# Kernel optimization log

Hardware: AMD Instinct MI355X
Metric: run time of the kernel (lower is better)

## Reference

```python
import jax, jax.numpy as jnp
import numpy as np

B, D, N, H = 16384, 8, 64, 128   # batch, input_path_dim, cde_state_dim, vf_hidden_dim
NSIG = D + D * (D - 1) // 2       # Lyndon words up to depth 2: letters + pairs i<j


def setup_inputs() -> dict:
    key = jax.random.key(0)
    ks = jax.random.split(key, 6)
    g = lambda k, shape, scale: jax.random.normal(k, shape, jnp.float32) * scale
    return {
        "h": jax.random.normal(ks[0], (B, N), jnp.float32),
        "primitive_signature": jax.random.normal(ks[1], (B, NSIG), jnp.float32) * 0.1,
        "W1": g(ks[2], (H, N), (1.0 / N) ** 0.5),
        "b1": jnp.zeros((H,), jnp.float32),
        "W2": g(ks[3], (H, H), (1.0 / H) ** 0.5),
        "b2": jnp.zeros((H,), jnp.float32),
        "W3": g(ks[4], (D * N, H), (1.0 / H) ** 0.5),
        "b3": jnp.zeros((D * N,), jnp.float32),
    }


def reference(h, primitive_signature, W1, b1, W2, b2, W3, b3):
    d, n = D, N
    iu, ju = np.triu_indices(d, k=1)  # level-2 Lyndon words ij with i<j, lex order

    def vf(hv):  # MLP vector field: (n,) -> (d, n), one field per input channel
        z = jax.nn.softplus(W1 @ hv + b1)
        z = jax.nn.softplus(W2 @ z + b2)
        return jnp.tanh(W3 @ z + b3).reshape(d, n)

    def single(hv, sig):
        V = vf(hv)  # (d, n) level-1 brackets (the vector fields themselves)
        # JVP of the whole stacked field in direction t: J_{V_j}(h) @ t for all j
        jvp_dir = lambda t: jax.jvp(vf, (hv,), (t,))[1]  # (d, n)
        JV = jax.vmap(jvp_dir)(V)                         # (i, j, n) = J_{V_j} V_i
        # Lie bracket [V_i, V_j](h) = J_{V_j} V_i - J_{V_i} V_j
        br2 = JV - jnp.swapaxes(JV, 0, 1)                 # (i, j, n)
        lyn2 = br2[iu, ju]                                # (d*(d-1)/2, n)
        # log-ODE contraction: sum_w logsig_w * bracket_w(h)
        return sig[:d] @ V + sig[d:] @ lyn2               # (n,)

    return jax.vmap(single)(h, primitive_signature)
```

## Files before the change

### kernel.cpp

```cpp
#include <hip/hip_runtime.h>
#include <hip/hip_bf16.h>

#define NEL 16384

#define W1B_OFF 0
#define W2B_OFF 8192
#define W3B_OFF 24576
#define WS_WEIGHTS 90112
#define S1_OFF  90112
#define S2_OFF  (S1_OFF + NEL*128)
#define Z2_OFF  (S2_OFF + NEL*128)
#define V_OFF   (Z2_OFF + NEL*128)
#define DZ1_OFF (V_OFF + NEL*512)
#define DZ2_OFF (DZ1_OFF + NEL*8*128)

typedef __attribute__((ext_vector_type(8))) short bf16x8;
typedef __attribute__((ext_vector_type(4))) float f32x4;

__device__ __forceinline__ float bf2f(unsigned int u16) {
    unsigned int x = u16 << 16;
    float f; __builtin_memcpy(&f, &x, 4); return f;
}
__device__ __forceinline__ unsigned short f2bf(float f) {
    unsigned int x; __builtin_memcpy(&x, &f, 4);
    x = (x + 0x7FFFu + ((x >> 16) & 1u)) >> 16;
    return (unsigned short)x;
}
__device__ __forceinline__ void unpack8(uint4 q, float* f) {
    f[0] = bf2f(q.x & 0xFFFFu); f[1] = bf2f(q.x >> 16);
    f[2] = bf2f(q.y & 0xFFFFu); f[3] = bf2f(q.y >> 16);
    f[4] = bf2f(q.z & 0xFFFFu); f[5] = bf2f(q.z >> 16);
    f[6] = bf2f(q.w & 0xFFFFu); f[7] = bf2f(q.w >> 16);
}
__device__ __forceinline__ void sp_sig(float x, float& sp, float& sig) {
    float t = __expf(-fabsf(x));
    float r = __builtin_amdgcn_rcpf(1.f + t);
    sig = (x >= 0.f) ? r : 1.f - r;
    sp  = fmaxf(x, 0.f) + __logf(1.f + t);
}
__device__ __forceinline__ float tanh_fast(float x) {
    float t = __expf(-2.f * fabsf(x));
    float y = (1.f - t) * __builtin_amdgcn_rcpf(1.f + t);
    unsigned int xb, yb;
    __builtin_memcpy(&xb, &x, 4);
    __builtin_memcpy(&yb, &y, 4);
    yb |= (xb & 0x80000000u);
    float rr; __builtin_memcpy(&rr, &yb, 4);
    return rr;
}
__device__ __forceinline__ bf16x8 ldfrag(const unsigned short* p) {
    return *reinterpret_cast<const bf16x8*>(p);
}
__device__ __forceinline__ void cpu4(unsigned short* dst, const unsigned short* src) {
    *reinterpret_cast<uint4*>(dst) = *reinterpret_cast<const uint4*>(src);
}

__global__ void prep_weights(const float* __restrict__ W1,
                             const float* __restrict__ W2,
                             const float* __restrict__ W3,
                             unsigned short* __restrict__ wb) {
    int i = blockIdx.x * blockDim.x + threadIdx.x;
    if (i >= WS_WEIGHTS) return;
    float v;
    if (i < W2B_OFF) v = W1[i];
    else if (i < W3B_OFF) v = W2[i - W2B_OFF];
    else v = W3[i - W3B_OFF];
    wb[i] = f2bf(v);
}

#define K1_LDS 39168
__global__ __launch_bounds__(256, 4)
void k1_fwd12(const float* __restrict__ hg,
              const float* __restrict__ b1,
              const float* __restrict__ b2,
              unsigned short* __restrict__ wsb) {
    __shared__ __align__(16) char sm[K1_LDS];
    unsigned short* w1s = (unsigned short*)(sm);
    unsigned short* hs  = (unsigned short*)(sm + 18432);
    unsigned short* w2s = (unsigned short*)(sm);
    unsigned short* z1s = (unsigned short*)(sm + 34816);
    unsigned short* S1g = wsb + S1_OFF;
    unsigned short* S2g = wsb + S2_OFF;
    unsigned short* Z2g = wsb + Z2_OFF;

    const int tid = threadIdx.x;
    const int e0 = blockIdx.x * 16;
    const int lane = tid & 63;
    const int w = tid >> 6;
    const int r16 = lane & 15;
    const int kb = lane >> 4;
    const int crow = kb * 4;

    #pragma unroll
    for (int q = 0; q < 4; ++q) {
        int idx = q * 256 + tid;
        int row = idx >> 3, u4 = idx & 7;
        cpu4(&w1s[row * 72 + u4 * 8], &wsb[W1B_OFF + row * 64 + u4 * 8]);
    }
    {
        int row = tid >> 4, f4 = tid & 15;
        float4 hv = *reinterpret_cast<const float4*>(&hg[(e0 + row) * 64 + f4 * 4]);
        ushort2 lo = { f2bf(hv.x), f2bf(hv.y) };
        ushort2 hi = { f2bf(hv.z), f2bf(hv.w) };
        *reinterpret_cast<ushort2*>(&hs[row * 72 + f4 * 4]) = lo;
        *reinterpret_cast<ushort2*>(&hs[row * 72 + f4 * 4 + 2]) = hi;
    }
    __syncthreads();

    {
        const unsigned short* Ab = hs + r16 * 72 + kb * 8;
        bf16x8 a0 = ldfrag(Ab), a1 = ldfrag(Ab + 32);
        f32x4 acc[2] = {};
        #pragma unroll
        for (int t = 0; t < 2; ++t) {
            int col16 = (w * 2 + t) * 16 + r16;
            const unsigned short* Bb = w1s + col16 * 72 + kb * 8;
            acc[t] = __builtin_amdgcn_mfma_f32_16x16x32_bf16(a0, ldfrag(Bb), acc[t], 0, 0, 0);
            acc[t] = __builtin_amdgcn_mfma_f32_16x16x32_bf16(a1, ldfrag(Bb + 32), acc[t], 0, 0, 0);
        }
        #pragma unroll
        for (int t = 0; t < 2; ++t) {
            int col = (w * 2 + t) * 16 + r16;
            float bb = b1[col];
            #pragma unroll
            for (int rr = 0; rr < 4; ++rr) {
                int e = crow + rr;
                float sp, sg;
                sp_sig(acc[t][rr] + bb, sp, sg);
                z1s[e * 136 + col] = f2bf(sp);
                S1g[(e0 + e) * 128 + col] = f2bf(sg);
            }
        }
    }
    __syncthreads();

    #pragma unroll
    for (int q = 0; q < 8; ++q) {
        int idx = q * 256 + tid;
        int row = idx >> 4, u4 = idx & 15;
        cpu4(&w2s[row * 136 + u4 * 8], &wsb[W2B_OFF + row * 128 + u4 * 8]);
    }
    __syncthreads();

    {
        const unsigned short* Ab = z1s + r16 * 136 + kb * 8;
        bf16x8 a[4];
        #pragma unroll
        for (int ks = 0; ks < 4; ++ks) a[ks] = ldfrag(Ab + ks * 32);
        f32x4 acc[2] = {};
        #pragma unroll
        for (int t = 0; t < 2; ++t) {
            int col16 = (w * 2 + t) * 16 + r16;
            const unsigned short* Bb = w2s + col16 * 136 + kb * 8;
            #pragma unroll
            for (int ks = 0; ks < 4; ++ks)
                acc[t] = __builtin_amdgcn_mfma_f32_16x16x32_bf16(a[ks], ldfrag(Bb + ks * 32), acc[t], 0, 0, 0);
        }
        #pragma unroll
        for (int t = 0; t < 2; ++t) {
            int col = (w * 2 + t) * 16 + r16;
            float bb = b2[col];
            #pragma unroll
            for (int rr = 0; rr < 4; ++rr) {
                int e = crow + rr;
                float sp, sg;
                sp_sig(acc[t][rr] + bb, sp, sg);
                Z2g[(e0 + e) * 128 + col] = f2bf(sp);
                S2g[(e0 + e) * 128 + col] = f2bf(sg);
            }
        }
    }
}

#define K2_LDS 39168
__global__ __launch_bounds__(256, 4)
void k2_fwd3(const float* __restrict__ b3,
             unsigned short* __restrict__ wsb) {
    __shared__ __align__(16) char sm[K2_LDS];
    unsigned short* z2s = (unsigned short*)(sm);
    unsigned short* wc  = (unsigned short*)(sm + 4352);
    const unsigned short* Z2g = wsb + Z2_OFF;
    unsigned short* Vg = wsb + V_OFF;

    const int tid = threadIdx.x;
    const int e0 = blockIdx.x * 16;
    const int lane = tid & 63;
    const int w = tid >> 6;
    const int r16 = lane & 15;
    const int kb = lane >> 4;
    const int crow = kb * 4;

    {
        int row = tid >> 4, u4 = tid & 15;
        cpu4(&z2s[row * 136 + u4 * 8], &Z2g[(e0 + row) * 128 + u4 * 8]);
    }

    for (int nc = 0; nc < 4; ++nc) {
        __syncthreads();
        #pragma unroll
        for (int q = 0; q < 8; ++q) {
            int idx = q * 256 + tid;
            int row = idx >> 4, u4 = idx & 15;
            cpu4(&wc[row * 136 + u4 * 8], &wsb[W3B_OFF + (nc * 128 + row) * 128 + u4 * 8]);
        }
        __syncthreads();

        const unsigned short* Ab = z2s + r16 * 136 + kb * 8;
        bf16x8 a[4];
        #pragma unroll
        for (int ks = 0; ks < 4; ++ks) a[ks] = ldfrag(Ab + ks * 32);
        f32x4 acc[2] = {};
        #pragma unroll
        for (int t = 0; t < 2; ++t) {
            int col16 = (w * 2 + t) * 16 + r16;
            const unsigned short* Bb = wc + col16 * 136 + kb * 8;
            #pragma unroll
            for (int ks = 0; ks < 4; ++ks)
                acc[t] = __builtin_amdgcn_mfma_f32_16x16x32_bf16(a[ks], ldfrag(Bb + ks * 32), acc[t], 0, 0, 0);
        }
        #pragma unroll
        for (int t = 0; t < 2; ++t) {
            int c = nc * 128 + (w * 2 + t) * 16 + r16;
            float bb = b3[c];
            #pragma unroll
            for (int rr = 0; rr < 4; ++rr) {
                int e = crow + rr;
                float v = tanh_fast(acc[t][rr] + bb);
                Vg[(e0 + e) * 512 + c] = f2bf(v);
            }
        }
    }
}

#define K3A_LDS 37120
__global__ __launch_bounds__(256, 4)
void k3a_jvp1(const float* __restrict__ sigg,
              unsigned short* __restrict__ wsb) {
    __shared__ __align__(16) char sm[K3A_LDS];
    unsigned short* vs  = (unsigned short*)(sm);
    unsigned short* w1s = (unsigned short*)(sm + 8320);
    unsigned short* ts  = (unsigned short*)(sm + 26752);
    float* sigsm = (float*)(sm + 35968);
    const unsigned short* S1g = wsb + S1_OFF;
    const unsigned short* Vg  = wsb + V_OFF;
    unsigned short* DZ1g = wsb + DZ1_OFF;

    const int tid = threadIdx.x;
    const int e0 = blockIdx.x * 8;
    const int lane = tid & 63;
    const int w = tid >> 6;
    const int r16 = lane & 15;
    const int kb = lane >> 4;

    #pragma unroll
    for (int q = 0; q < 2; ++q) {
        int idx = q * 256 + tid;
        int row = idx >> 6, u4 = idx & 63;
        cpu4(&vs[row * 520 + u4 * 8], &Vg[(e0 + row) * 512 + u4 * 8]);
    }
    #pragma unroll
    for (int q = 0; q < 4; ++q) {
        int idx = q * 256 + tid;
        int row = idx >> 3, u4 = idx & 7;
        cpu4(&w1s[row * 72 + u4 * 8], &wsb[W1B_OFF + row * 64 + u4 * 8]);
    }
    #pragma unroll
    for (int q = 0; q < 2; ++q) {
        int idx = q * 256 + tid;
        if (idx < 288) sigsm[idx] = sigg[e0 * 36 + idx];
    }
    __syncthreads();

    {
        int m = tid >> 2, kq = tid & 3;
        int e = m >> 3, j = m & 7;
        float c8[8];
        #pragma unroll
        for (int i = 0; i < 8; ++i) {
            float v = 0.f;
            if (i < j) {
                int p = 7 * i - i * (i - 1) / 2 + (j - i - 1);
                v = sigsm[e * 36 + 8 + p];
            } else if (i > j) {
                int p = 7 * j - j * (j - 1) / 2 + (i - j - 1);
                v = -sigsm[e * 36 + 8 + p];
            }
            c8[i] = v;
        }
        float acc[16] = {};
        #pragma unroll
        for (int i = 0; i < 8; ++i) {
            uint4 qa = *reinterpret_cast<const uint4*>(&vs[e * 520 + i * 64 + kq * 16]);
            uint4 qb = *reinterpret_cast<const uint4*>(&vs[e * 520 + i * 64 + kq * 16 + 8]);
            float fa[8], fb[8];
            unpack8(qa, fa); unpack8(qb, fb);
            #pragma unroll
            for (int kk = 0; kk < 8; ++kk) {
                acc[kk]     += c8[i] * fa[kk];
                acc[kk + 8] += c8[i] * fb[kk];
            }
        }
        unsigned short o[16];
        #pragma unroll
        for (int kk = 0; kk < 16; ++kk) o[kk] = f2bf(acc[kk]);
        uint4 qo;
        qo.x = (unsigned int)o[0] | ((unsigned int)o[1] << 16);
        qo.y = (unsigned int)o[2] | ((unsigned int)o[3] << 16);
        qo.z = (unsigned int)o[4] | ((unsigned int)o[5] << 16);
        qo.w = (unsigned int)o[6] | ((unsigned int)o[7] << 16);
        *reinterpret_cast<uint4*>(&ts[m * 72 + kq * 16]) = qo;
        qo.x = (unsigned int)o[8]  | ((unsigned int)o[9]  << 16);
        qo.y = (unsigned int)o[10] | ((unsigned int)o[11] << 16);
        qo.z = (unsigned int)o[12] | ((unsigned int)o[13] << 16);
        qo.w = (unsigned int)o[14] | ((unsigned int)o[15] << 16);
        *reinterpret_cast<uint4*>(&ts[m * 72 + kq * 16 + 8]) = qo;
    }
    __syncthreads();

    {
        const unsigned short* Ab = ts + (w * 16 + r16) * 72 + kb * 8;
        bf16x8 a0 = ldfrag(Ab), a1 = ldfrag(Ab + 32);
        f32x4 acc[8] = {};
        #pragma unroll
        for (int nt = 0; nt < 8; ++nt) {
            const unsigned short* Bb = w1s + (nt * 16 + r16) * 72 + kb * 8;
            acc[nt] = __builtin_amdgcn_mfma_f32_16x16x32_bf16(a0, ldfrag(Bb), acc[nt], 0, 0, 0);
            acc[nt] = __builtin_amdgcn_mfma_f32_16x16x32_bf16(a1, ldfrag(Bb + 32), acc[nt], 0, 0, 0);
        }
        int rbase = w * 16 + kb * 4;
        int e_loc = rbase >> 3;
        #pragma unroll
        for (int nt = 0; nt < 8; ++nt) {
            int col = nt * 16 + r16;
            float s1v = bf2f(S1g[(e0 + e_loc) * 128 + col]);
            #pragma unroll
            for (int rr = 0; rr < 4; ++rr)
                DZ1g[(e0 * 8 + rbase + rr) * 128 + col] = f2bf(acc[nt][rr] * s1v);
        }
    }
}

#define K3B_LDS 43520
__global__ __launch_bounds__(256, 3)
void k3b_jvp2(unsigned short* __restrict__ wsb) {
    __shared__ __align__(16) char sm[K3B_LDS];
    unsigned short* dz1s = (unsigned short*)(sm);
    unsigned short* w2s  = (unsigned short*)(sm + 8704);
    const unsigned short* S2g = wsb + S2_OFF;
    const unsigned short* DZ1g = wsb + DZ1_OFF;
    unsigned short* DZ2g = wsb + DZ2_OFF;

    const int tid = threadIdx.x;
    const int m0 = blockIdx.x * 32;
    const int lane = tid & 63;
    const int w = tid >> 6;
    const int r16 = lane & 15;
    const int kb = lane >> 4;
    const int mt = w & 1, nh = w >> 1;

    #pragma unroll
    for (int q = 0; q < 2; ++q) {
        int idx = q * 256 + tid;
        int row = idx >> 4, u4 = idx & 15;
        cpu4(&dz1s[row * 136 + u4 * 8], &DZ1g[(m0 + row) * 128 + u4 * 8]);
    }
    #pragma unroll
    for (int q = 0; q < 8; ++q) {
        int idx = q * 256 + tid;
        int row = idx >> 4, u4 = idx & 15;
        cpu4(&w2s[row * 136 + u4 * 8], &wsb[W2B_OFF + row * 128 + u4 * 8]);
    }
    __syncthreads();

    const unsigned short* Ab = dz1s + (mt * 16 + r16) * 136 + kb * 8;
    bf16x8 a[4];
    #pragma unroll
    for (int ks = 0; ks < 4; ++ks) a[ks] = ldfrag(Ab + ks * 32);
    f32x4 acc[4] = {};
    #pragma unroll
    for (int nt = 0; nt < 4; ++nt) {
        const unsigned short* Bb = w2s + ((nh * 4 + nt) * 16 + r16) * 136 + kb * 8;
        #pragma unroll
        for (int ks = 0; ks < 4; ++ks)
            acc[nt] = __builtin_amdgcn_mfma_f32_16x16x32_bf16(a[ks], ldfrag(Bb + ks * 32), acc[nt], 0, 0, 0);
    }
    int rbase = mt * 16 + kb * 4;
    int e_glob = (m0 + rbase) >> 3;
    #pragma unroll
    for (int nt = 0; nt < 4; ++nt) {
        int col = (nh * 4 + nt) * 16 + r16;
        float s2v = bf2f(S2g[e_glob * 128 + col]);
        #pragma unroll
        for (int rr = 0; rr < 4; ++rr)
            DZ2g[(m0 + rbase + rr) * 128 + col] = f2bf(acc[nt][rr] * s2v);
    }
}

#define K4_LDS 22336
__global__ __launch_bounds__(256, 4)
void k4_jvp3(const float* __restrict__ sigg,
             const unsigned short* __restrict__ wsb,
             float* __restrict__ out) {
    __shared__ __align__(16) char sm[K4_LDS];
    unsigned short* adz = (unsigned short*)(sm);
    unsigned short* w3j = (unsigned short*)(sm + 4352);
    float*          sg1 = (float*)(sm + 21760);
    const unsigned short* Vg = wsb + V_OFF;
    const unsigned short* DZ2g = wsb + DZ2_OFF;

    const int tid = threadIdx.x;
    const int e0 = blockIdx.x * 16;
    const int lane = tid & 63;
    const int w = tid >> 6;
    const int r16 = lane & 15;
    const int kb = lane >> 4;
    const int crow = kb * 4;
    const int np = w * 16 + r16;

    if (tid < 128) {
        int e = tid >> 3, j7 = tid & 7;
        sg1[e * 9 + j7] = sigg[(e0 + e) * 36 + j7];
    }

    float oacc[4] = {};

    for (int j = 0; j < 8; ++j) {
        __syncthreads();
        {
            int row = tid >> 4, u4 = tid & 15;
            cpu4(&adz[row * 136 + u4 * 8], &DZ2g[((e0 + row) * 8 + j) * 128 + u4 * 8]);
        }
        #pragma unroll
        for (int q = 0; q < 4; ++q) {
            int idx = q * 256 + tid;
            int row = idx >> 4, u4 = idx & 15;
            cpu4(&w3j[row * 136 + u4 * 8], &wsb[W3B_OFF + (j * 64 + row) * 128 + u4 * 8]);
        }
        __syncthreads();

        const unsigned short* Ab = adz + r16 * 136 + kb * 8;
        bf16x8 a[4];
        #pragma unroll
        for (int ks = 0; ks < 4; ++ks) a[ks] = ldfrag(Ab + ks * 32);
        f32x4 acc = {};
        const unsigned short* Bb = w3j + np * 136 + kb * 8;
        #pragma unroll
        for (int ks = 0; ks < 4; ++ks)
            acc = __builtin_amdgcn_mfma_f32_16x16x32_bf16(a[ks], ldfrag(Bb + ks * 32), acc, 0, 0, 0);

        #pragma unroll
        for (int rr = 0; rr < 4; ++rr) {
            int e = crow + rr;
            float v = bf2f(Vg[(e0 + e) * 512 + j * 64 + np]);
            float sv = sg1[e * 9 + j];
            oacc[rr] += sv * v + (1.f - v * v) * acc[rr];
        }
    }

    #pragma unroll
    for (int rr = 0; rr < 4; ++rr)
        out[(e0 + crow + rr) * 64 + np] = oacc[rr];
}

extern "C" void kernel_launch(void* const* d_in, const int* in_sizes, int n_in,
                              void* d_out, int out_size, void* d_ws, size_t ws_size,
                              hipStream_t stream) {
    const float* hg  = (const float*)d_in[0];
    const float* sg  = (const float*)d_in[1];
    const float* W1  = (const float*)d_in[2];
    const float* b1  = (const float*)d_in[3];
    const float* W2  = (const float*)d_in[4];
    const float* b2  = (const float*)d_in[5];
    const float* W3  = (const float*)d_in[6];
    const float* b3  = (const float*)d_in[7];
    float* outp = (float*)d_out;
    unsigned short* wsb = (unsigned short*)d_ws;

    hipLaunchKernelGGL(prep_weights, dim3((WS_WEIGHTS + 255) / 256), dim3(256), 0, stream,
                       W1, W2, W3, wsb);
    hipLaunchKernelGGL(k1_fwd12, dim3(NEL / 16), dim3(256), 0, stream, hg, b1, b2, wsb);
    hipLaunchKernelGGL(k2_fwd3,  dim3(NEL / 16), dim3(256), 0, stream, b3, wsb);
    hipLaunchKernelGGL(k3a_jvp1, dim3(NEL / 8),  dim3(256), 0, stream, sg, wsb);
    hipLaunchKernelGGL(k3b_jvp2, dim3(NEL * 8 / 32), dim3(256), 0, stream, wsb);
    hipLaunchKernelGGL(k4_jvp3,  dim3(NEL / 16), dim3(256), 0, stream, sg, wsb, outp);
}
```

Baseline: 78.30 us.

## Fuse forward layers and JVP stages to drop intermediate global round-trips

Merges the layer-1/2 forward kernel with the layer-3 forward kernel, so Z2 stays in shared memory instead of going through global memory. Merges the two JVP kernels so DZ1 is kept in registers and shared memory rather than written to and reread from the workspace. In the last kernel, W3 slices are double-buffered and the DZ2 fragments are read straight from global memory. Fewer launches and less intermediate traffic, at the cost of larger shared-memory footprint and lower occupancy in the fused JVP kernel.

```diff
diff --git a/kernel.cpp b/kernel.cpp
--- a/kernel.cpp
+++ b/kernel.cpp
@@ -9,10 +9,8 @@
 #define WS_WEIGHTS 90112
 #define S1_OFF  90112
 #define S2_OFF  (S1_OFF + NEL*128)
-#define Z2_OFF  (S2_OFF + NEL*128)
-#define V_OFF   (Z2_OFF + NEL*128)
-#define DZ1_OFF (V_OFF + NEL*512)
-#define DZ2_OFF (DZ1_OFF + NEL*8*128)
+#define V_OFF   (S2_OFF + NEL*128)
+#define DZ2_OFF (V_OFF + NEL*512)
 
 typedef __attribute__((ext_vector_type(8))) short bf16x8;
 typedef __attribute__((ext_vector_type(4))) float f32x4;
@@ -68,20 +66,23 @@
     wb[i] = f2bf(v);
 }
 
-#define K1_LDS 39168
+#define K12_LDS 39168
 __global__ __launch_bounds__(256, 4)
-void k1_fwd12(const float* __restrict__ hg,
-              const float* __restrict__ b1,
-              const float* __restrict__ b2,
-              unsigned short* __restrict__ wsb) {
-    __shared__ __align__(16) char sm[K1_LDS];
+void k12_fwd(const float* __restrict__ hg,
+             const float* __restrict__ b1,
+             const float* __restrict__ b2,
+             const float* __restrict__ b3,
+             unsigned short* __restrict__ wsb) {
+    __shared__ __align__(16) char sm[K12_LDS];
     unsigned short* w1s = (unsigned short*)(sm);
     unsigned short* hs  = (unsigned short*)(sm + 18432);
     unsigned short* w2s = (unsigned short*)(sm);
+    unsigned short* wc  = (unsigned short*)(sm);
     unsigned short* z1s = (unsigned short*)(sm + 34816);
+    unsigned short* z2s = (unsigned short*)(sm + 34816);
     unsigned short* S1g = wsb + S1_OFF;
     unsigned short* S2g = wsb + S2_OFF;
-    unsigned short* Z2g = wsb + Z2_OFF;
+    unsigned short* Vg  = wsb + V_OFF;
 
     const int tid = threadIdx.x;
     const int e0 = blockIdx.x * 16;
@@ -147,6 +148,7 @@
         bf16x8 a[4];
         #pragma unroll
         for (int ks = 0; ks < 4; ++ks) a[ks] = ldfrag(Ab + ks * 32);
+        __syncthreads();
         f32x4 acc[2] = {};
         #pragma unroll
         for (int t = 0; t < 2; ++t) {
@@ -165,34 +167,10 @@
                 int e = crow + rr;
                 float sp, sg;
                 sp_sig(acc[t][rr] + bb, sp, sg);
-                Z2g[(e0 + e) * 128 + col] = f2bf(sp);
+                z2s[e * 136 + col] = f2bf(sp);
                 S2g[(e0 + e) * 128 + col] = f2bf(sg);
             }
         }
-    }
-}
-
-#define K2_LDS 39168
-__global__ __launch_bounds__(256, 4)
-void k2_fwd3(const float* __restrict__ b3,
-             unsigned short* __restrict__ wsb) {
-    __shared__ __align__(16) char sm[K2_LDS];
-    unsigned short* z2s = (unsigned short*)(sm);
-    unsigned short* wc  = (unsigned short*)(sm + 4352);
-    const unsigned short* Z2g = wsb + Z2_OFF;
-    unsigned short* Vg = wsb + V_OFF;
-
-    const int tid = threadIdx.x;
-    const int e0 = blockIdx.x * 16;
-    const int lane = tid & 63;
-    const int w = tid >> 6;
-    const int r16 = lane & 15;
-    const int kb = lane >> 4;
-    const int crow = kb * 4;
-
-    {
-        int row = tid >> 4, u4 = tid & 15;
-        cpu4(&z2s[row * 136 + u4 * 8], &Z2g[(e0 + row) * 128 + u4 * 8]);
     }
 
     for (int nc = 0; nc < 4; ++nc) {
@@ -232,18 +210,21 @@
     }
 }
 
-#define K3A_LDS 37120
-__global__ __launch_bounds__(256, 4)
-void k3a_jvp1(const float* __restrict__ sigg,
+#define K3_LDS 53376
+__global__ __launch_bounds__(256, 3)
+void k3_jvp12(const float* __restrict__ sigg,
               unsigned short* __restrict__ wsb) {
-    __shared__ __align__(16) char sm[K3A_LDS];
-    unsigned short* vs  = (unsigned short*)(sm);
-    unsigned short* w1s = (unsigned short*)(sm + 8320);
-    unsigned short* ts  = (unsigned short*)(sm + 26752);
-    float* sigsm = (float*)(sm + 35968);
+    __shared__ __align__(16) char sm[K3_LDS];
+    unsigned short* vs   = (unsigned short*)(sm);
+    unsigned short* w1s  = (unsigned short*)(sm + 8320);
+    unsigned short* ts   = (unsigned short*)(sm + 26752);
+    unsigned short* dz1s = (unsigned short*)(sm);
+    unsigned short* w2s  = (unsigned short*)(sm + 17408);
+    float* sigsm = (float*)(sm + 52224);
     const unsigned short* S1g = wsb + S1_OFF;
+    const unsigned short* S2g = wsb + S2_OFF;
     const unsigned short* Vg  = wsb + V_OFF;
-    unsigned short* DZ1g = wsb + DZ1_OFF;
+    unsigned short* DZ2g = wsb + DZ2_OFF;
 
     const int tid = threadIdx.x;
     const int e0 = blockIdx.x * 8;
@@ -317,6 +298,9 @@
     }
     __syncthreads();
 
+    float dz1v[8][4];
+    const int rbase = w * 16 + kb * 4;
+    const int e_loc = rbase >> 3;
     {
         const unsigned short* Ab = ts + (w * 16 + r16) * 72 + kb * 8;
         bf16x8 a0 = ldfrag(Ab), a1 = ldfrag(Ab + 32);
@@ -327,42 +311,23 @@
             acc[nt] = __builtin_amdgcn_mfma_f32_16x16x32_bf16(a0, ldfrag(Bb), acc[nt], 0, 0, 0);
             acc[nt] = __builtin_amdgcn_mfma_f32_16x16x32_bf16(a1, ldfrag(Bb + 32), acc[nt], 0, 0, 0);
         }
-        int rbase = w * 16 + kb * 4;
-        int e_loc = rbase >> 3;
         #pragma unroll
         for (int nt = 0; nt < 8; ++nt) {
             int col = nt * 16 + r16;
             float s1v = bf2f(S1g[(e0 + e_loc) * 128 + col]);
             #pragma unroll
             for (int rr = 0; rr < 4; ++rr)
-                DZ1g[(e0 * 8 + rbase + rr) * 128 + col] = f2bf(acc[nt][rr] * s1v);
-        }
-    }
-}
-
-#define K3B_LDS 43520
-__global__ __launch_bounds__(256, 3)
-void k3b_jvp2(unsigned short* __restrict__ wsb) {
-    __shared__ __align__(16) char sm[K3B_LDS];
-    unsigned short* dz1s = (unsigned short*)(sm);
-    unsigned short* w2s  = (unsigned short*)(sm + 8704);
-    const unsigned short* S2g = wsb + S2_OFF;
-    const unsigned short* DZ1g = wsb + DZ1_OFF;
-    unsigned short* DZ2g = wsb + DZ2_OFF;
-
-    const int tid = threadIdx.x;
-    const int m0 = blockIdx.x * 32;
-    const int lane = tid & 63;
-    const int w = tid >> 6;
-    const int r16 = lane & 15;
-    const int kb = lane >> 4;
-    const int mt = w & 1, nh = w >> 1;
-
-    #pragma unroll
-    for (int q = 0; q < 2; ++q) {
-        int idx = q * 256 + tid;
-        int row = idx >> 4, u4 = idx & 15;
-        cpu4(&dz1s[row * 136 + u4 * 8], &DZ1g[(m0 + row) * 128 + u4 * 8]);
+                dz1v[nt][rr] = acc[nt][rr] * s1v;
+        }
+    }
+    __syncthreads();
+
+    #pragma unroll
+    for (int nt = 0; nt < 8; ++nt) {
+        int col = nt * 16 + r16;
+        #pragma unroll
+        for (int rr = 0; rr < 4; ++rr)
+            dz1s[(rbase + rr) * 136 + col] = f2bf(dz1v[nt][rr]);
     }
     #pragma unroll
     for (int q = 0; q < 8; ++q) {
@@ -372,39 +337,39 @@
     }
     __syncthreads();
 
-    const unsigned short* Ab = dz1s + (mt * 16 + r16) * 136 + kb * 8;
-    bf16x8 a[4];
-    #pragma unroll
-    for (int ks = 0; ks < 4; ++ks) a[ks] = ldfrag(Ab + ks * 32);
-    f32x4 acc[4] = {};
-    #pragma unroll
-    for (int nt = 0; nt < 4; ++nt) {
-        const unsigned short* Bb = w2s + ((nh * 4 + nt) * 16 + r16) * 136 + kb * 8;
-        #pragma unroll
-        for (int ks = 0; ks < 4; ++ks)
-            acc[nt] = __builtin_amdgcn_mfma_f32_16x16x32_bf16(a[ks], ldfrag(Bb + ks * 32), acc[nt], 0, 0, 0);
-    }
-    int rbase = mt * 16 + kb * 4;
-    int e_glob = (m0 + rbase) >> 3;
-    #pragma unroll
-    for (int nt = 0; nt < 4; ++nt) {
-        int col = (nh * 4 + nt) * 16 + r16;
-        float s2v = bf2f(S2g[e_glob * 128 + col]);
-        #pragma unroll
-        for (int rr = 0; rr < 4; ++rr)
-            DZ2g[(m0 + rbase + rr) * 128 + col] = f2bf(acc[nt][rr] * s2v);
-    }
-}
-
-#define K4_LDS 22336
+    {
+        const unsigned short* Ab = dz1s + (w * 16 + r16) * 136 + kb * 8;
+        bf16x8 a[4];
+        #pragma unroll
+        for (int ks = 0; ks < 4; ++ks) a[ks] = ldfrag(Ab + ks * 32);
+        f32x4 acc[8] = {};
+        #pragma unroll
+        for (int nt = 0; nt < 8; ++nt) {
+            const unsigned short* Bb = w2s + (nt * 16 + r16) * 136 + kb * 8;
+            #pragma unroll
+            for (int ks = 0; ks < 4; ++ks)
+                acc[nt] = __builtin_amdgcn_mfma_f32_16x16x32_bf16(a[ks], ldfrag(Bb + ks * 32), acc[nt], 0, 0, 0);
+        }
+        #pragma unroll
+        for (int nt = 0; nt < 8; ++nt) {
+            int col = nt * 16 + r16;
+            float s2v = bf2f(S2g[(e0 + e_loc) * 128 + col]);
+            #pragma unroll
+            for (int rr = 0; rr < 4; ++rr)
+                DZ2g[(e0 * 8 + rbase + rr) * 128 + col] = f2bf(acc[nt][rr] * s2v);
+        }
+    }
+}
+
+#define K4_LDS 35392
 __global__ __launch_bounds__(256, 4)
 void k4_jvp3(const float* __restrict__ sigg,
              const unsigned short* __restrict__ wsb,
              float* __restrict__ out) {
     __shared__ __align__(16) char sm[K4_LDS];
-    unsigned short* adz = (unsigned short*)(sm);
-    unsigned short* w3j = (unsigned short*)(sm + 4352);
-    float*          sg1 = (float*)(sm + 21760);
+    unsigned short* w3j0 = (unsigned short*)(sm);
+    unsigned short* w3j1 = (unsigned short*)(sm + 17408);
+    float*          sg1  = (float*)(sm + 34816);
     const unsigned short* Vg = wsb + V_OFF;
     const unsigned short* DZ2g = wsb + DZ2_OFF;
 
@@ -421,29 +386,34 @@
         int e = tid >> 3, j7 = tid & 7;
         sg1[e * 9 + j7] = sigg[(e0 + e) * 36 + j7];
     }
+    #pragma unroll
+    for (int q = 0; q < 4; ++q) {
+        int idx = q * 256 + tid;
+        int row = idx >> 4, u4 = idx & 15;
+        cpu4(&w3j0[row * 136 + u4 * 8], &wsb[W3B_OFF + row * 128 + u4 * 8]);
+    }
+    __syncthreads();
 
     float oacc[4] = {};
+    const unsigned short* Agbase = DZ2g + (e0 + r16) * 8 * 128 + kb * 8;
 
     for (int j = 0; j < 8; ++j) {
-        __syncthreads();
-        {
-            int row = tid >> 4, u4 = tid & 15;
-            cpu4(&adz[row * 136 + u4 * 8], &DZ2g[((e0 + row) * 8 + j) * 128 + u4 * 8]);
-        }
-        #pragma unroll
-        for (int q = 0; q < 4; ++q) {
-            int idx = q * 256 + tid;
-            int row = idx >> 4, u4 = idx & 15;
-            cpu4(&w3j[row * 136 + u4 * 8], &wsb[W3B_OFF + (j * 64 + row) * 128 + u4 * 8]);
-        }
-        __syncthreads();
-
-        const unsigned short* Ab = adz + r16 * 136 + kb * 8;
+        unsigned short* cur = (j & 1) ? w3j1 : w3j0;
+        unsigned short* nxt = (j & 1) ? w3j0 : w3j1;
+        if (j < 7) {
+            #pragma unroll
+            for (int q = 0; q < 4; ++q) {
+                int idx = q * 256 + tid;
+                int row = idx >> 4, u4 = idx & 15;
+                cpu4(&nxt[row * 136 + u4 * 8], &wsb[W3B_OFF + ((j + 1) * 64 + row) * 128 + u4 * 8]);
+            }
+        }
+        const unsigned short* Ag = Agbase + j * 128;
         bf16x8 a[4];
         #pragma unroll
-        for (int ks = 0; ks < 4; ++ks) a[ks] = ldfrag(Ab + ks * 32);
+        for (int ks = 0; ks < 4; ++ks) a[ks] = ldfrag(Ag + ks * 32);
         f32x4 acc = {};
-        const unsigned short* Bb = w3j + np * 136 + kb * 8;
+        const unsigned short* Bb = cur + np * 136 + kb * 8;
         #pragma unroll
         for (int ks = 0; ks < 4; ++ks)
             acc = __builtin_amdgcn_mfma_f32_16x16x32_bf16(a[ks], ldfrag(Bb + ks * 32), acc, 0, 0, 0);
@@ -455,6 +425,7 @@
             float sv = sg1[e * 9 + j];
             oacc[rr] += sv * v + (1.f - v * v) * acc[rr];
         }
+        __syncthreads();
     }
 
     #pragma unroll
@@ -478,9 +449,7 @@
 
     hipLaunchKernelGGL(prep_weights, dim3((WS_WEIGHTS + 255) / 256), dim3(256), 0, stream,
                        W1, W2, W3, wsb);
-    hipLaunchKernelGGL(k1_fwd12, dim3(NEL / 16), dim3(256), 0, stream, hg, b1, b2, wsb);
-    hipLaunchKernelGGL(k2_fwd3,  dim3(NEL / 16), dim3(256), 0, stream, b3, wsb);
-    hipLaunchKernelGGL(k3a_jvp1, dim3(NEL / 8),  dim3(256), 0, stream, sg, wsb);
-    hipLaunchKernelGGL(k3b_jvp2, dim3(NEL * 8 / 32), dim3(256), 0, stream, wsb);
-    hipLaunchKernelGGL(k4_jvp3,  dim3(NEL / 16), dim3(256), 0, stream, sg, wsb, outp);
-}
+    hipLaunchKernelGGL(k12_fwd, dim3(NEL / 16), dim3(256), 0, stream, hg, b1, b2, b3, wsb);
+    hipLaunchKernelGGL(k3_jvp12, dim3(NEL / 8), dim3(256), 0, stream, sg, wsb);
+    hipLaunchKernelGGL(k4_jvp3, dim3(NEL / 16), dim3(256), 0, stream, sg, wsb, outp);
+}
```

After: 76.29 us. 1.03x faster.
